# Kernel optimization log

Measured on AMD Instinct MI355X. Metric: run time of the kernel, lower is better.

The kernel has to match this reference:

```python
import jax, jax.numpy as jnp
import numpy as np


def gcn_conv(x, row, col, ew, W, b, N):
    # GCNConv: add self-loops (weight 1), symmetric normalization, X @ W, scatter-add, + bias
    loop = jnp.arange(N, dtype=row.dtype)
    r = jnp.concatenate([row, loop])
    c = jnp.concatenate([col, loop])
    w = jnp.concatenate([ew, jnp.ones((N,), dtype=x.dtype)])
    deg = jax.ops.segment_sum(w, c, num_segments=N)
    dinv = jnp.where(deg > 0, jax.lax.rsqrt(deg), 0.0).astype(x.dtype)
    norm = dinv[r] * w * dinv[c]                  # [E+N]
    h = x @ W                                     # [N, out]
    msg = h[r] * norm[:, None]                    # gather + scale
    out = jax.ops.segment_sum(msg, c, num_segments=N)  # scatter-add to targets
    return out + b


def setup_inputs() -> dict:
    key = jax.random.key(0)
    ks = jax.random.split(key, 10)
    N, E, C_in, C_hid, C_out = 65536, 1048576, 16, 64, 2
    x = jax.random.normal(ks[0], (N, C_in), dtype=jnp.float32)
    edge_index = jax.random.randint(ks[1], (2, E), 0, N, dtype=jnp.int64)
    edge_weight = jax.random.uniform(ks[2], (E,), dtype=jnp.float32)
    s = lambda k, sh, fan: jax.random.normal(k, sh, dtype=jnp.float32) / np.sqrt(fan)
    return {
        "x": x,
        "edge_index": edge_index,
        "edge_weight": edge_weight,
        "W1": s(ks[3], (C_in, C_hid), C_in),
        "b1": jnp.zeros((C_hid,), dtype=jnp.float32),
        "W2": s(ks[4], (C_hid, C_hid), C_hid),
        "b2": jnp.zeros((C_hid,), dtype=jnp.float32),
        "Wl": s(ks[5], (C_hid, C_out), C_hid),
        "bl": jnp.zeros((C_out,), dtype=jnp.float32),
    }


def reference(x, edge_index, edge_weight, W1, b1, W2, b2, Wl, bl):
    N = x.shape[0]
    row, col = edge_index[0], edge_index[1]  # source -> target
    h = jax.nn.relu(gcn_conv(x, row, col, edge_weight, W1, b1, N))
    h = jax.nn.relu(gcn_conv(h, row, col, edge_weight, W2, b2, N))
    return h @ Wl + bl
```

## Files before the change

kernel.cpp:

```cpp
#include <hip/hip_runtime.h>
#include <hip/hip_fp16.h>

#define NSB 1024

__device__ __forceinline__ unsigned pack_h2(float a, float b) {
    __half2 h = __floats2half2_rn(a, b);
    return *reinterpret_cast<unsigned*>(&h);
}

__global__ __launch_bounds__(256) void s1_hist(const int* __restrict__ col,
                                               int* __restrict__ F, int E, int chunk) {
    __shared__ int cnt[256];
    int t = threadIdx.x, b = blockIdx.x;
    cnt[t] = 0;
    __syncthreads();
    int s = b * chunk, e = min(E, s + chunk);
    for (int i = s + t; i < e; i += 256) atomicAdd(&cnt[col[i] >> 8], 1);
    __syncthreads();
    F[t * NSB + b] = cnt[t];
}

__global__ void scanF1(int* __restrict__ F, int* __restrict__ bsum, int n) {
    __shared__ int sd[256];
    int t = threadIdx.x, i = blockIdx.x * 256 + t;
    int v = (i < n) ? F[i] : 0;
    sd[t] = v;
    __syncthreads();
    for (int o = 1; o < 256; o <<= 1) {
        int x = (t >= o) ? sd[t - o] : 0;
        __syncthreads();
        sd[t] += x;
        __syncthreads();
    }
    if (i < n) F[i] = sd[t] - v;
    if (t == 255) bsum[blockIdx.x] = sd[255];
}

__global__ void scanF2(const int* __restrict__ bsum, int* __restrict__ boff, int nb) {
    __shared__ int sd[1024];
    int t = threadIdx.x;
    int v = (t < nb) ? bsum[t] : 0;
    sd[t] = v;
    __syncthreads();
    for (int o = 1; o < 1024; o <<= 1) {
        int x = (t >= o) ? sd[t - o] : 0;
        __syncthreads();
        sd[t] += x;
        __syncthreads();
    }
    if (t < nb) boff[t] = sd[t] - v;
}

__global__ void scanF3(int* __restrict__ F, const int* __restrict__ boff, int n) {
    int i = blockIdx.x * blockDim.x + threadIdx.x;
    if (i < n) F[i] += boff[i >> 8];
}

__global__ __launch_bounds__(256) void s3_scatter(const int* __restrict__ col,
                                                  const int* __restrict__ row,
                                                  const float* __restrict__ ew,
                                                  const int* __restrict__ F,
                                                  int2* __restrict__ tmp, int E, int chunk) {
    __shared__ int off[256];
    __shared__ int cur[256];
    int t = threadIdx.x, b = blockIdx.x;
    off[t] = F[t * NSB + b];
    cur[t] = 0;
    __syncthreads();
    int s = b * chunk, e = min(E, s + chunk);
    for (int i = s + t; i < e; i += 256) {
        int c = col[i];
        int bk = c >> 8;
        int rk = atomicAdd(&cur[bk], 1);
        tmp[off[bk] + rk] = make_int2(row[i] | ((c & 255) << 16), __float_as_int(ew[i]));
    }
}

__global__ __launch_bounds__(256) void s4_fine(const int2* __restrict__ tmp,
                                               const int* __restrict__ F,
                                               unsigned* __restrict__ pack,
                                               float* __restrict__ dinv,
                                               int* __restrict__ start,
                                               const float* __restrict__ x,
                                               const float* __restrict__ W1,
                                               __half* __restrict__ g1,
                                               int n, int E, int nbuck) {
    __shared__ int   fcnt[256];
    __shared__ float fdeg[256];
    __shared__ int   foff[256];
    __shared__ int   fcur[256];
    __shared__ float Ws[16 * 64];
    int t = threadIdx.x, b = blockIdx.x;
    reinterpret_cast<float4*>(Ws)[t] = reinterpret_cast<const float4*>(W1)[t];
    fcnt[t] = 0; fdeg[t] = 0.f; fcur[t] = 0;
    __syncthreads();
    int segS = F[b * NSB];
    int segE = (b == nbuck - 1) ? E : F[(b + 1) * NSB];
    for (int i = segS + t; i < segE; i += 256) {
        int2 v = tmp[i];
        int f = (v.x >> 16) & 255;
        atomicAdd(&fcnt[f], 1);
        atomicAdd(&fdeg[f], __int_as_float(v.y));
    }
    __syncthreads();
    int val = fcnt[t];
    foff[t] = val;
    __syncthreads();
    for (int o = 1; o < 256; o <<= 1) {
        int xk = (t >= o) ? foff[t - o] : 0;
        __syncthreads();
        foff[t] += xk;
        __syncthreads();
    }
    int excl = foff[t] - val;
    int c = (b << 8) | t;
    float di = rsqrtf(fdeg[t] + 1.0f);
    if (c < n) {
        dinv[c]  = di;
        start[c] = segS + excl;
    }
    if (b == nbuck - 1 && t == 255) start[n] = E;
    __syncthreads();
    foff[t] = excl;
    __syncthreads();
    for (int i = segS + t; i < segE; i += 256) {
        int2 v = tmp[i];
        int f = (v.x >> 16) & 255;
        int rk = atomicAdd(&fcur[f], 1);
        __half hw = __float2half_rn(__int_as_float(v.y));
        pack[segS + foff[f] + rk] =
            (unsigned)(v.x & 0xFFFF) | ((unsigned)*reinterpret_cast<unsigned short*>(&hw) << 16);
    }
    if (c >= n) return;
    float xv[16];
    const float4* xr = reinterpret_cast<const float4*>(x + (size_t)c * 16);
#pragma unroll
    for (int i = 0; i < 4; ++i)
        *reinterpret_cast<float4*>(&xv[i * 4]) = xr[i];
    uint2* orow = reinterpret_cast<uint2*>(g1 + ((size_t)c << 6));
    for (int jb = 0; jb < 16; ++jb) {
        float4 acc = make_float4(0.f, 0.f, 0.f, 0.f);
#pragma unroll
        for (int k = 0; k < 16; ++k) {
            float hk = xv[k];
            const float4 wv = *reinterpret_cast<const float4*>(&Ws[k * 64 + jb * 4]);
            acc.x += hk * wv.x; acc.y += hk * wv.y;
            acc.z += hk * wv.z; acc.w += hk * wv.w;
        }
        uint2 st;
        st.x = pack_h2(acc.x * di, acc.y * di);
        st.y = pack_h2(acc.z * di, acc.w * di);
        orow[jb] = st;
    }
}

__global__ __launch_bounds__(256) void gemm_hid(const float* __restrict__ h,
                                                const float* __restrict__ W,
                                                const float* __restrict__ dinv,
                                                __half* __restrict__ out, int n) {
    __shared__ float Ws[64 * 64];
    int t = threadIdx.x;
#pragma unroll
    for (int i = 0; i < 16; ++i) Ws[i * 256 + t] = W[i * 256 + t];
    __syncthreads();
    int node = blockIdx.x * 256 + t;
    if (node >= n) return;
    float hv[64];
    const float4* hr = reinterpret_cast<const float4*>(h + ((size_t)node << 6));
#pragma unroll
    for (int i = 0; i < 16; ++i)
        *reinterpret_cast<float4*>(&hv[i * 4]) = hr[i];
    float di = dinv[node];
    uint2* orow = reinterpret_cast<uint2*>(out + ((size_t)node << 6));
    for (int jb = 0; jb < 16; ++jb) {
        float4 acc = make_float4(0.f, 0.f, 0.f, 0.f);
#pragma unroll
        for (int k = 0; k < 64; ++k) {
            float hk = hv[k];
            const float4 wv = *reinterpret_cast<const float4*>(&Ws[k * 64 + jb * 4]);
            acc.x += hk * wv.x; acc.y += hk * wv.y;
            acc.z += hk * wv.z; acc.w += hk * wv.w;
        }
        uint2 st;
        st.x = pack_h2(acc.x * di, acc.y * di);
        st.y = pack_h2(acc.z * di, acc.w * di);
        orow[jb] = st;
    }
}

__device__ __forceinline__ float4 load_row4(const __half* __restrict__ g,
                                            unsigned pk, int ch4, float* wout) {
    unsigned short hw = (unsigned short)(pk >> 16);
    *wout = __half2float(*reinterpret_cast<__half*>(&hw));
    uint2 u = *reinterpret_cast<const uint2*>(g + ((size_t)(pk & 0xFFFFu) << 6) + ch4);
    float2 a = __half22float2(*reinterpret_cast<__half2*>(&u.x));
    float2 b = __half22float2(*reinterpret_cast<__half2*>(&u.y));
    return make_float4(a.x, a.y, b.x, b.y);
}

__device__ __forceinline__ float4 gather_acc(const int* __restrict__ start,
                                             const unsigned* __restrict__ pack,
                                             const __half* __restrict__ g,
                                             int wid, int sub, int ch4) {
    int s = start[wid], e = start[wid + 1];
    float4 acc = make_float4(0.f, 0.f, 0.f, 0.f);
    int i = s;
    for (; i + 7 < e; i += 8) {
        unsigned pa = pack[i + sub];
        unsigned pb = pack[i + 4 + sub];
        float wa, wb;
        float4 va = load_row4(g, pa, ch4, &wa);
        float4 vb = load_row4(g, pb, ch4, &wb);
        acc.x += va.x * wa; acc.y += va.y * wa; acc.z += va.z * wa; acc.w += va.w * wa;
        acc.x += vb.x * wb; acc.y += vb.y * wb; acc.z += vb.z * wb; acc.w += vb.w * wb;
    }
    if (i + 3 < e) {
        unsigned pa = pack[i + sub];
        float wa;
        float4 va = load_row4(g, pa, ch4, &wa);
        acc.x += va.x * wa; acc.y += va.y * wa; acc.z += va.z * wa; acc.w += va.w * wa;
        i += 4;
    }
    int rem = e - i;
    if (sub < rem) {
        unsigned pa = pack[i + sub];
        float wa;
        float4 va = load_row4(g, pa, ch4, &wa);
        acc.x += va.x * wa; acc.y += va.y * wa; acc.z += va.z * wa; acc.w += va.w * wa;
    }
#pragma unroll
    for (int m = 16; m <= 32; m <<= 1) {
        acc.x += __shfl_xor(acc.x, m, 64);
        acc.y += __shfl_xor(acc.y, m, 64);
        acc.z += __shfl_xor(acc.z, m, 64);
        acc.w += __shfl_xor(acc.w, m, 64);
    }
    return acc;
}

__global__ __launch_bounds__(256) void gather_mid(const int* __restrict__ start,
                                                  const unsigned* __restrict__ pack,
                                                  const __half* __restrict__ g,
                                                  const float* __restrict__ dinv,
                                                  const float* __restrict__ b,
                                                  float* __restrict__ out, int n) {
    int wid = (blockIdx.x * blockDim.x + threadIdx.x) >> 6;
    if (wid >= n) return;
    int lane = threadIdx.x & 63;
    int sub = lane >> 4;
    int ch4 = (lane & 15) << 2;
    float4 acc = gather_acc(start, pack, g, wid, sub, ch4);
    if (sub == 0) {
        float di = dinv[wid];
        uint2 u0 = *reinterpret_cast<const uint2*>(g + ((size_t)wid << 6) + ch4);
        float2 ga = __half22float2(*reinterpret_cast<__half2*>(&u0.x));
        float2 gb = __half22float2(*reinterpret_cast<__half2*>(&u0.y));
        const float4 bb = *reinterpret_cast<const float4*>(b + ch4);
        float4 r;
        r.x = fmaxf(di * (acc.x + ga.x) + bb.x, 0.f);
        r.y = fmaxf(di * (acc.y + ga.y) + bb.y, 0.f);
        r.z = fmaxf(di * (acc.z + gb.x) + bb.z, 0.f);
        r.w = fmaxf(di * (acc.w + gb.y) + bb.w, 0.f);
        *reinterpret_cast<float4*>(out + ((size_t)wid << 6) + ch4) = r;
    }
}

__global__ __launch_bounds__(256) void gather_head(const int* __restrict__ start,
                                                   const unsigned* __restrict__ pack,
                                                   const __half* __restrict__ g,
                                                   const float* __restrict__ dinv,
                                                   const float* __restrict__ b,
                                                   const float* __restrict__ Wl,
                                                   const float* __restrict__ bl,
                                                   float* __restrict__ out, int n) {
    int wid = (blockIdx.x * blockDim.x + threadIdx.x) >> 6;
    if (wid >= n) return;
    int lane = threadIdx.x & 63;
    int sub = lane >> 4;
    int ch4 = (lane & 15) << 2;
    float4 acc = gather_acc(start, pack, g, wid, sub, ch4);
    if (sub == 0) {
        float di = dinv[wid];
        uint2 u0 = *reinterpret_cast<const uint2*>(g + ((size_t)wid << 6) + ch4);
        float2 ga = __half22float2(*reinterpret_cast<__half2*>(&u0.x));
        float2 gb = __half22float2(*reinterpret_cast<__half2*>(&u0.y));
        const float4 bb = *reinterpret_cast<const float4*>(b + ch4);
        float4 h;
        h.x = fmaxf(di * (acc.x + ga.x) + bb.x, 0.f);
        h.y = fmaxf(di * (acc.y + ga.y) + bb.y, 0.f);
        h.z = fmaxf(di * (acc.z + gb.x) + bb.z, 0.f);
        h.w = fmaxf(di * (acc.w + gb.y) + bb.w, 0.f);
        float s0 = h.x * Wl[(ch4 + 0) * 2] + h.y * Wl[(ch4 + 1) * 2] +
                   h.z * Wl[(ch4 + 2) * 2] + h.w * Wl[(ch4 + 3) * 2];
        float s1 = h.x * Wl[(ch4 + 0) * 2 + 1] + h.y * Wl[(ch4 + 1) * 2 + 1] +
                   h.z * Wl[(ch4 + 2) * 2 + 1] + h.w * Wl[(ch4 + 3) * 2 + 1];
#pragma unroll
        for (int m = 1; m <= 8; m <<= 1) {
            s0 += __shfl_xor(s0, m, 64);
            s1 += __shfl_xor(s1, m, 64);
        }
        if (lane == 0) {
            out[(size_t)wid * 2 + 0] = s0 + bl[0];
            out[(size_t)wid * 2 + 1] = s1 + bl[1];
        }
    }
}

extern "C" void kernel_launch(void* const* d_in, const int* in_sizes, int n_in,
                              void* d_out, int out_size, void* d_ws, size_t ws_size,
                              hipStream_t stream) {
    const float* x  = (const float*)d_in[0];
    const int*   ei = (const int*)d_in[1];
    const float* ew = (const float*)d_in[2];
    const float* W1 = (const float*)d_in[3];
    const float* b1 = (const float*)d_in[4];
    const float* W2 = (const float*)d_in[5];
    const float* b2 = (const float*)d_in[6];
    const float* Wl = (const float*)d_in[7];
    const float* bl = (const float*)d_in[8];
    float* out = (float*)d_out;

    const int N = in_sizes[0] / 16;
    const int E = in_sizes[2];
    const int* row = ei;
    const int* col = ei + E;
    const int NB    = (N + 255) / 256;
    const int nbuck = N >> 8;
    const int chunk = (E + NSB - 1) / NSB;
    const int FSZ   = nbuck * NSB;
    const int FB    = (FSZ + 255) / 256;

    char* p = (char*)d_ws;
    unsigned* pack = (unsigned*)p;  p += (size_t)E * 4;
    __half*   bufA = (__half*)p;    p += (size_t)N * 64 * 2;
    char*     r2   = p;             p += (size_t)N * 64 * 4;
    float*    dinv = (float*)p;     p += (size_t)N * 4;
    int*    startO = (int*)p;       p += (size_t)(N + 1) * 4;

    int2* tmp  = (int2*)r2;
    int*  F    = (int*)(r2 + (size_t)E * 8);
    int*  bsum = F + FSZ;
    int*  boff = bsum + FB;
    float* bufB = (float*)r2;

    s1_hist<<<NSB, 256, 0, stream>>>(col, F, E, chunk);
    scanF1<<<FB, 256, 0, stream>>>(F, bsum, FSZ);
    scanF2<<<1, 1024, 0, stream>>>(bsum, boff, FB);
    scanF3<<<FB, 256, 0, stream>>>(F, boff, FSZ);
    s3_scatter<<<NSB, 256, 0, stream>>>(col, row, ew, F, tmp, E, chunk);
    s4_fine<<<nbuck, 256, 0, stream>>>(tmp, F, pack, dinv, startO, x, W1, bufA, N, E, nbuck);

    gather_mid<<<(N + 3) / 4, 256, 0, stream>>>(startO, pack, bufA, dinv, b1, bufB, N);

    gemm_hid<<<NB, 256, 0, stream>>>(bufB, W2, dinv, bufA, N);

    gather_head<<<(N + 3) / 4, 256, 0, stream>>>(startO, pack, bufA, dinv, b2, Wl, bl, out, N);
}
```

Measured before the change: 138.7 us.

## Stage edge chunks in LDS for coalesced bucket scatter and fuse scan passes

Each scatter block now works on a fixed 4096-edge chunk. It loads the chunk into shared memory, sorts it locally by coarse bucket and writes contiguous runs, instead of issuing random global writes. The fine-sort kernel likewise stages its segment in LDS (up to 6144 edges) and writes the packed output in order, with a global-memory fallback for larger segments. The two follow-up scan kernels are removed, and each block recomputes the 256-entry block offsets itself. This cuts launches and uncoalesced writes at the cost of extra LDS use, which lowers occupancy, plus redundant per-block scans.

```diff
diff --git a/kernel.cpp b/kernel.cpp
--- a/kernel.cpp
+++ b/kernel.cpp
@@ -1,23 +1,42 @@
 #include <hip/hip_runtime.h>
 #include <hip/hip_fp16.h>
 
-#define NSB 1024
+#define CHUNK 4096
+#define SEGCAP 6144
 
 __device__ __forceinline__ unsigned pack_h2(float a, float b) {
     __half2 h = __floats2half2_rn(a, b);
     return *reinterpret_cast<unsigned*>(&h);
 }
 
+__device__ __forceinline__ void scan_boff(const int* __restrict__ bsum, int nb,
+                                          int* boff) {
+    int t = threadIdx.x;
+    int v = (t < nb) ? bsum[t] : 0;
+    boff[t] = v;
+    __syncthreads();
+    for (int o = 1; o < 256; o <<= 1) {
+        int x = (t >= o) ? boff[t - o] : 0;
+        __syncthreads();
+        boff[t] += x;
+        __syncthreads();
+    }
+    int excl = boff[t] - v;
+    __syncthreads();
+    boff[t] = excl;
+    __syncthreads();
+}
+
 __global__ __launch_bounds__(256) void s1_hist(const int* __restrict__ col,
-                                               int* __restrict__ F, int E, int chunk) {
+                                               int* __restrict__ F, int E, int nsb) {
     __shared__ int cnt[256];
     int t = threadIdx.x, b = blockIdx.x;
     cnt[t] = 0;
     __syncthreads();
-    int s = b * chunk, e = min(E, s + chunk);
+    int s = b * CHUNK, e = min(E, s + CHUNK);
     for (int i = s + t; i < e; i += 256) atomicAdd(&cnt[col[i] >> 8], 1);
     __syncthreads();
-    F[t * NSB + b] = cnt[t];
+    F[t * nsb + b] = cnt[t];
 }
 
 __global__ void scanF1(int* __restrict__ F, int* __restrict__ bsum, int n) {
@@ -36,101 +55,156 @@
     if (t == 255) bsum[blockIdx.x] = sd[255];
 }
 
-__global__ void scanF2(const int* __restrict__ bsum, int* __restrict__ boff, int nb) {
-    __shared__ int sd[1024];
-    int t = threadIdx.x;
-    int v = (t < nb) ? bsum[t] : 0;
-    sd[t] = v;
-    __syncthreads();
-    for (int o = 1; o < 1024; o <<= 1) {
-        int x = (t >= o) ? sd[t - o] : 0;
-        __syncthreads();
-        sd[t] += x;
-        __syncthreads();
-    }
-    if (t < nb) boff[t] = sd[t] - v;
-}
-
-__global__ void scanF3(int* __restrict__ F, const int* __restrict__ boff, int n) {
-    int i = blockIdx.x * blockDim.x + threadIdx.x;
-    if (i < n) F[i] += boff[i >> 8];
-}
-
 __global__ __launch_bounds__(256) void s3_scatter(const int* __restrict__ col,
                                                   const int* __restrict__ row,
                                                   const float* __restrict__ ew,
                                                   const int* __restrict__ F,
-                                                  int2* __restrict__ tmp, int E, int chunk) {
+                                                  const int* __restrict__ bsum,
+                                                  int2* __restrict__ tmp, int E, int nsb) {
+    __shared__ int boff[256];
     __shared__ int off[256];
+    __shared__ int cnt[256];
+    __shared__ int lofs[256];
     __shared__ int cur[256];
+    __shared__ int2 ed[CHUNK];
+    __shared__ unsigned short perm[CHUNK];
     int t = threadIdx.x, b = blockIdx.x;
-    off[t] = F[t * NSB + b];
-    cur[t] = 0;
-    __syncthreads();
-    int s = b * chunk, e = min(E, s + chunk);
-    for (int i = s + t; i < e; i += 256) {
-        int c = col[i];
-        int bk = c >> 8;
+    scan_boff(bsum, nsb, boff);
+    off[t] = F[t * nsb + b] + boff[t];
+    cnt[t] = 0; cur[t] = 0;
+    __syncthreads();
+    int s = b * CHUNK;
+    int m = min(E - s, CHUNK);
+    for (int i = t; i < m; i += 256) {
+        int c = col[s + i];
+        ed[i] = make_int2((row[s + i] & 0xFFFF) | (c << 16), __float_as_int(ew[s + i]));
+        atomicAdd(&cnt[c >> 8], 1);
+    }
+    __syncthreads();
+    int v = cnt[t];
+    lofs[t] = v;
+    __syncthreads();
+    for (int o = 1; o < 256; o <<= 1) {
+        int x = (t >= o) ? lofs[t - o] : 0;
+        __syncthreads();
+        lofs[t] += x;
+        __syncthreads();
+    }
+    int excl = lofs[t] - v;
+    __syncthreads();
+    lofs[t] = excl;
+    __syncthreads();
+    for (int i = t; i < m; i += 256) {
+        int bk = ((unsigned)ed[i].x) >> 24;
         int rk = atomicAdd(&cur[bk], 1);
-        tmp[off[bk] + rk] = make_int2(row[i] | ((c & 255) << 16), __float_as_int(ew[i]));
+        perm[lofs[bk] + rk] = (unsigned short)i;
+    }
+    __syncthreads();
+    for (int p = t; p < m; p += 256) {
+        int2 v2 = ed[perm[p]];
+        int bk = ((unsigned)v2.x) >> 24;
+        tmp[off[bk] + (p - lofs[bk])] = v2;
     }
 }
 
 __global__ __launch_bounds__(256) void s4_fine(const int2* __restrict__ tmp,
                                                const int* __restrict__ F,
+                                               const int* __restrict__ bsum,
                                                unsigned* __restrict__ pack,
                                                float* __restrict__ dinv,
                                                int* __restrict__ start,
                                                const float* __restrict__ x,
                                                const float* __restrict__ W1,
                                                __half* __restrict__ g1,
-                                               int n, int E, int nbuck) {
+                                               int n, int E, int nsb, int nbuck) {
+    __shared__ int   boff[256];
     __shared__ int   fcnt[256];
     __shared__ float fdeg[256];
     __shared__ int   foff[256];
     __shared__ int   fcur[256];
     __shared__ float Ws[16 * 64];
+    __shared__ int2  seg[SEGCAP];
+    __shared__ unsigned short perm[SEGCAP];
     int t = threadIdx.x, b = blockIdx.x;
+    scan_boff(bsum, nsb, boff);
     reinterpret_cast<float4*>(Ws)[t] = reinterpret_cast<const float4*>(W1)[t];
     fcnt[t] = 0; fdeg[t] = 0.f; fcur[t] = 0;
     __syncthreads();
-    int segS = F[b * NSB];
-    int segE = (b == nbuck - 1) ? E : F[(b + 1) * NSB];
-    for (int i = segS + t; i < segE; i += 256) {
-        int2 v = tmp[i];
-        int f = (v.x >> 16) & 255;
-        atomicAdd(&fcnt[f], 1);
-        atomicAdd(&fdeg[f], __int_as_float(v.y));
-    }
-    __syncthreads();
-    int val = fcnt[t];
-    foff[t] = val;
-    __syncthreads();
-    for (int o = 1; o < 256; o <<= 1) {
-        int xk = (t >= o) ? foff[t - o] : 0;
-        __syncthreads();
-        foff[t] += xk;
-        __syncthreads();
-    }
-    int excl = foff[t] - val;
+    int segS = F[b * nsb] + boff[b];
+    int segE = (b == nbuck - 1) ? E : (F[(b + 1) * nsb] + boff[b + 1]);
+    int m = segE - segS;
+    if (m <= SEGCAP) {
+        for (int i = t; i < m; i += 256) seg[i] = tmp[segS + i];
+        __syncthreads();
+        for (int i = t; i < m; i += 256) {
+            int2 v = seg[i];
+            int f = (v.x >> 16) & 255;
+            atomicAdd(&fcnt[f], 1);
+            atomicAdd(&fdeg[f], __int_as_float(v.y));
+        }
+        __syncthreads();
+        int val = fcnt[t];
+        foff[t] = val;
+        __syncthreads();
+        for (int o = 1; o < 256; o <<= 1) {
+            int xk = (t >= o) ? foff[t - o] : 0;
+            __syncthreads();
+            foff[t] += xk;
+            __syncthreads();
+        }
+        int excl = foff[t] - val;
+        __syncthreads();
+        foff[t] = excl;
+        __syncthreads();
+        for (int i = t; i < m; i += 256) {
+            int f = (seg[i].x >> 16) & 255;
+            int rk = atomicAdd(&fcur[f], 1);
+            perm[foff[f] + rk] = (unsigned short)i;
+        }
+        __syncthreads();
+        for (int p = t; p < m; p += 256) {
+            int2 v = seg[perm[p]];
+            __half hw = __float2half_rn(__int_as_float(v.y));
+            pack[segS + p] = (unsigned)(v.x & 0xFFFF) |
+                             ((unsigned)*reinterpret_cast<unsigned short*>(&hw) << 16);
+        }
+    } else {
+        for (int i = segS + t; i < segE; i += 256) {
+            int2 v = tmp[i];
+            int f = (v.x >> 16) & 255;
+            atomicAdd(&fcnt[f], 1);
+            atomicAdd(&fdeg[f], __int_as_float(v.y));
+        }
+        __syncthreads();
+        int val = fcnt[t];
+        foff[t] = val;
+        __syncthreads();
+        for (int o = 1; o < 256; o <<= 1) {
+            int xk = (t >= o) ? foff[t - o] : 0;
+            __syncthreads();
+            foff[t] += xk;
+            __syncthreads();
+        }
+        int excl = foff[t] - val;
+        __syncthreads();
+        foff[t] = excl;
+        __syncthreads();
+        for (int i = segS + t; i < segE; i += 256) {
+            int2 v = tmp[i];
+            int f = (v.x >> 16) & 255;
+            int rk = atomicAdd(&fcur[f], 1);
+            __half hw = __float2half_rn(__int_as_float(v.y));
+            pack[segS + foff[f] + rk] = (unsigned)(v.x & 0xFFFF) |
+                             ((unsigned)*reinterpret_cast<unsigned short*>(&hw) << 16);
+        }
+    }
     int c = (b << 8) | t;
     float di = rsqrtf(fdeg[t] + 1.0f);
     if (c < n) {
         dinv[c]  = di;
-        start[c] = segS + excl;
+        start[c] = segS + foff[t];
     }
     if (b == nbuck - 1 && t == 255) start[n] = E;
-    __syncthreads();
-    foff[t] = excl;
-    __syncthreads();
-    for (int i = segS + t; i < segE; i += 256) {
-        int2 v = tmp[i];
-        int f = (v.x >> 16) & 255;
-        int rk = atomicAdd(&fcur[f], 1);
-        __half hw = __float2half_rn(__int_as_float(v.y));
-        pack[segS + foff[f] + rk] =
-            (unsigned)(v.x & 0xFFFF) | ((unsigned)*reinterpret_cast<unsigned short*>(&hw) << 16);
-    }
     if (c >= n) return;
     float xv[16];
     const float4* xr = reinterpret_cast<const float4*>(x + (size_t)c * 16);
@@ -326,8 +400,8 @@
     const int* col = ei + E;
     const int NB    = (N + 255) / 256;
     const int nbuck = N >> 8;
-    const int chunk = (E + NSB - 1) / NSB;
-    const int FSZ   = nbuck * NSB;
+    const int nsb   = (E + CHUNK - 1) / CHUNK;
+    const int FSZ   = 256 * nsb;
     const int FB    = (FSZ + 255) / 256;
 
     char* p = (char*)d_ws;
@@ -340,15 +414,13 @@
     int2* tmp  = (int2*)r2;
     int*  F    = (int*)(r2 + (size_t)E * 8);
     int*  bsum = F + FSZ;
-    int*  boff = bsum + FB;
     float* bufB = (float*)r2;
 
-    s1_hist<<<NSB, 256, 0, stream>>>(col, F, E, chunk);
+    s1_hist<<<nsb, 256, 0, stream>>>(col, F, E, nsb);
     scanF1<<<FB, 256, 0, stream>>>(F, bsum, FSZ);
-    scanF2<<<1, 1024, 0, stream>>>(bsum, boff, FB);
-    scanF3<<<FB, 256, 0, stream>>>(F, boff, FSZ);
-    s3_scatter<<<NSB, 256, 0, stream>>>(col, row, ew, F, tmp, E, chunk);
-    s4_fine<<<nbuck, 256, 0, stream>>>(tmp, F, pack, dinv, startO, x, W1, bufA, N, E, nbuck);
+    s3_scatter<<<nsb, 256, 0, stream>>>(col, row, ew, F, bsum, tmp, E, nsb);
+    s4_fine<<<nbuck, 256, 0, stream>>>(tmp, F, bsum, pack, dinv, startO,
+                                       x, W1, bufA, N, E, nsb, nbuck);
 
     gather_mid<<<(N + 3) / 4, 256, 0, stream>>>(startO, pack, bufA, dinv, b1, bufB, N);
 
```

Measured after the change: 137.7 us, median of 2. No clear change (-0.7%).
